# Optimization experiments

Measured on AMD Instinct MI355X. Metric: run time of the kernel, lower is better.

The kernel has to match this reference:

```python
import jax, jax.numpy as jnp
import numpy as np

B, NV, RN, SN = 1, 4, 1024, 128
H = W = 256
C_FEAT = 32   # img_feat_dim
D_VIEW = 32   # view transformer d_model
PE_D = 8      # PE_d_hid
D_RAY = D_VIEW + PE_D  # 40
NHEAD = 8
EPS_LN = 1e-5


def _layernorm(x, g, b):
    m = x.mean(-1, keepdims=True)
    v = ((x - m) ** 2).mean(-1, keepdims=True)
    return (x - m) * jax.lax.rsqrt(v + EPS_LN) * g + b


def _linear_attention(q, k, v):
    # LoFTR kernelized linear attention; q,k,v: (n, L, h, d)
    Q = jax.nn.elu(q) + 1.0
    K = jax.nn.elu(k) + 1.0
    L = v.shape[1]
    KV = jnp.einsum('nshd,nshv->nhdv', K, v / L)
    Z = 1.0 / (jnp.einsum('nlhd,nhd->nlh', Q, K.sum(axis=1)) + 1e-6)
    return jnp.einsum('nlhd,nhdv,nlh->nlhv', Q, KV, Z) * L


def _loftr_self_layer(x, Wq, Wk, Wv, Wm, g1, b1, W1, W2, g2, b2):
    # LoFTREncoderLayer with self-attention (x is both query and source)
    n, L, d = x.shape
    dim = d // NHEAD
    q = (x @ Wq).reshape(n, L, NHEAD, dim)
    k = (x @ Wk).reshape(n, L, NHEAD, dim)
    v = (x @ Wv).reshape(n, L, NHEAD, dim)
    msg = _linear_attention(q, k, v).reshape(n, L, d) @ Wm
    msg = _layernorm(msg, g1, b1)
    msg = jax.nn.relu(jnp.concatenate([x, msg], -1) @ W1) @ W2
    msg = _layernorm(msg, g2, b2)
    return x + msg


def _grid_sample_2d(img, pix):
    # img: (N,C,H,W); pix: (N,RN,SN,2) in pixel coords.
    # bilinear, align_corners=True, zero padding; mask = in-bounds.
    N, C, Hh, Ww = img.shape
    x, y = pix[..., 0], pix[..., 1]
    mask = ((x >= 0) & (x <= Ww - 1) & (y >= 0) & (y <= Hh - 1)).astype(img.dtype)
    x0 = jnp.floor(x)
    y0 = jnp.floor(y)
    flat = img.reshape(N, C, Hh * Ww)

    def gather(ix, iy):
        valid = ((ix >= 0) & (ix < Ww) & (iy >= 0) & (iy < Hh)).astype(img.dtype)
        idx = (jnp.clip(iy, 0, Hh - 1) * Ww + jnp.clip(ix, 0, Ww - 1)).astype(jnp.int32)
        out = jnp.take_along_axis(flat, idx.reshape(N, 1, -1), axis=2)
        return out.reshape(N, C, ix.shape[1], ix.shape[2]) * valid[:, None]

    wx1 = x - x0
    wy1 = y - y0
    out = (gather(x0, y0) * ((1 - wx1) * (1 - wy1))[:, None]
           + gather(x0 + 1, y0) * (wx1 * (1 - wy1))[:, None]
           + gather(x0, y0 + 1) * ((1 - wx1) * wy1)[:, None]
           + gather(x0 + 1, y0 + 1) * (wx1 * wy1)[:, None])
    return out, mask


def _order_posenc(d_hid, n):
    pos = np.arange(n)[:, None].astype(np.float64)
    j = np.arange(d_hid)[None, :]
    tab = pos / np.power(10000.0, 2 * (j // 2) / d_hid)
    tab[:, 0::2] = np.sin(tab[:, 0::2])
    tab[:, 1::2] = np.cos(tab[:, 1::2])
    return jnp.asarray(tab, dtype=jnp.float32)


def _forward(point3D, source_imgs, source_imgs_feat, ref_pose_inv, source_poses_inv,
             source_poses, view_token,
             vt_Wq, vt_Wk, vt_Wv, vt_Wm, vt_g1, vt_b1, vt_W1, vt_W2, vt_g2, vt_b2,
             rt_Wq, rt_Wk, rt_Wv, rt_Wm, rt_g1, rt_b1, rt_W1, rt_W2, rt_g2, rt_b2,
             dm_W1, dm_b1, dm_W2, dm_b2, dm_W3, dm_b3,
             rw_W1, rw_b1, rw_W2, rw_b2, rw_W3, rw_b3):
    b, nv, _, h, w = source_imgs.shape
    _, rn, sn, _ = point3D.shape

    # relative viewing directions (B,NV,RN,SN,3)
    v1 = point3D - ref_pose_inv[:, None, None, :3, -1]
    v2 = point3D[:, None] - source_poses_inv[:, :, None, None, :3, -1]
    v1 = v1 / jnp.linalg.norm(v1, axis=-1, keepdims=True)
    v2 = v2 / jnp.linalg.norm(v2, axis=-1, keepdims=True)
    dir_relative = v1[:, None] - v2

    # project points into all source views: (B,NV,3,RN,SN)
    pts_h = jnp.concatenate([point3D, jnp.ones_like(point3D[..., :1])], -1)
    pip = jnp.einsum('bnij,brsj->bnirs', source_poses, pts_h)[:, :, :3]
    mask_valid_depth = (pip[:, :, 2] > 0).astype(point3D.dtype)
    pix = pip[:, :, :2] / pip[:, :, 2:3]
    grid = jnp.moveaxis(pix, 2, -1).reshape(b * nv, rn, sn, 2)

    feat_s, mask = _grid_sample_2d(source_imgs_feat.reshape(b * nv, -1, h, w), grid)
    rgb_s, _ = _grid_sample_2d(source_imgs.reshape(b * nv, -1, h, w), grid)
    mask = mask.reshape(b, nv, rn, sn) * mask_valid_depth

    # per-point multi-view tokens: (B*RN*SN, NV, C)
    x = feat_s.reshape(b, nv, -1, rn, sn).transpose(0, 3, 4, 1, 2).reshape(b * rn * sn, nv, -1)
    tok = jnp.broadcast_to(view_token, (x.shape[0], 1, view_token.shape[-1]))
    x = jnp.concatenate([tok, x], axis=1)  # prepend view token -> L = NV+1
    x = _loftr_self_layer(x, vt_Wq, vt_Wk, vt_Wv, vt_Wm, vt_g1, vt_b1, vt_W1, vt_W2, vt_g2, vt_b2)

    x1 = jnp.moveaxis(x, 1, 0)          # (NV+1, B*RN*SN, C)
    view_feature = x1[1:]
    x = x1[0].reshape(b * rn, sn, -1)   # token output per sample along ray

    pe = _order_posenc(PE_D, sn)        # (SN, 8)
    x = jnp.concatenate([x, jnp.broadcast_to(pe, (b * rn, sn, PE_D))], -1)
    x = _loftr_self_layer(x, rt_Wq, rt_Wk, rt_Wv, rt_Wm, rt_g1, rt_b1, rt_W1, rt_W2, rt_g2, rt_b2)

    hdm = jax.nn.relu(x @ dm_W1 + dm_b1)
    hdm = jax.nn.relu(hdm @ dm_W2 + dm_b2)
    srdf = hdm @ dm_W3 + dm_b3           # (B*RN, SN, 1)

    # radiance blending weights over views
    vf = view_feature.reshape(nv, b, rn, sn, -1).transpose(1, 2, 3, 0, 4)  # (B,RN,SN,NV,C)
    dr = dir_relative.transpose(0, 2, 3, 1, 4)                             # (B,RN,SN,NV,3)
    xw = jnp.concatenate([vf, dr], -1)
    xw = jax.nn.relu(xw @ rw_W1 + rw_b1)
    xw = jax.nn.relu(xw @ rw_W2 + rw_b2)
    xw = xw @ rw_W3 + rw_b3                                                # (B,RN,SN,NV,1)
    m = mask.transpose(0, 2, 3, 1)[..., None]
    xw = jnp.where(m == 0, -1e9, xw)
    weight = jax.nn.softmax(xw, axis=-2)
    w_bn = weight[..., 0].transpose(0, 3, 1, 2)[:, :, None]                # (B,NV,1,RN,SN)
    radiance = (rgb_s.reshape(b, nv, 3, rn, sn) * w_bn).sum(axis=1)        # (B,3,RN,SN)
    radiance = radiance.transpose(0, 2, 3, 1).reshape(b * rn * sn, 3)
    return radiance, srdf, pip


def setup_inputs() -> dict:
    key = jax.random.key(0)
    ks = jax.random.split(key, 4)
    u = jax.random.uniform(ks[0], (B, RN, SN, 3), dtype=jnp.float32)
    point3D = jnp.concatenate([u[..., :2] - 0.5, u[..., 2:] + 1.0], -1)  # x,y in [-.5,.5], z in [1,2]
    source_imgs = jax.random.normal(ks[1], (B, NV, 3, H, W), dtype=jnp.float32) * 0.5
    source_imgs_feat = jax.random.normal(ks[2], (B, NV, C_FEAT, H, W), dtype=jnp.float32) * 0.5

    f = 200.0
    P = np.array([[f, 0, W / 2, 0], [0, f, H / 2, 0], [0, 0, 1, 0], [0, 0, 0, 1]], np.float32)
    source_poses = jnp.asarray(np.broadcast_to(P, (B, NV, 4, 4)).copy())
    ref_pose_inv = jnp.asarray(np.broadcast_to(np.eye(4, dtype=np.float32), (B, 4, 4)).copy())
    spi = np.broadcast_to(np.eye(4, dtype=np.float32), (B, NV, 4, 4)).copy()
    spi[:, :, 0, 3] = np.linspace(-0.2, 0.2, NV, dtype=np.float32)  # camera centers
    source_poses_inv = jnp.asarray(spi)

    pk = jax.random.split(ks[3], 20)

    def lin(k, i, o):
        return jax.random.normal(k, (i, o), dtype=jnp.float32) * 0.05

    d, dr = D_VIEW, D_RAY
    params = dict(
        view_token=jax.random.normal(pk[0], (1, d), dtype=jnp.float32),
        vt_Wq=lin(pk[1], d, d), vt_Wk=lin(pk[2], d, d), vt_Wv=lin(pk[3], d, d), vt_Wm=lin(pk[4], d, d),
        vt_g1=jnp.ones(d), vt_b1=jnp.zeros(d),
        vt_W1=lin(pk[5], 2 * d, 2 * d), vt_W2=lin(pk[6], 2 * d, d),
        vt_g2=jnp.ones(d), vt_b2=jnp.zeros(d),
        rt_Wq=lin(pk[7], dr, dr), rt_Wk=lin(pk[8], dr, dr), rt_Wv=lin(pk[9], dr, dr), rt_Wm=lin(pk[10], dr, dr),
        rt_g1=jnp.ones(dr), rt_b1=jnp.zeros(dr),
        rt_W1=lin(pk[11], 2 * dr, 2 * dr), rt_W2=lin(pk[12], 2 * dr, dr),
        rt_g2=jnp.ones(dr), rt_b2=jnp.zeros(dr),
        dm_W1=lin(pk[13], dr, 32), dm_b1=jnp.zeros(32),
        dm_W2=lin(pk[14], 32, 16), dm_b2=jnp.zeros(16),
        dm_W3=lin(pk[15], 16, 1), dm_b3=jnp.zeros(1),
        rw_W1=lin(pk[16], d + 3, 16), rw_b1=jnp.zeros(16),
        rw_W2=lin(pk[17], 16, 8), rw_b2=jnp.zeros(8),
        rw_W3=lin(pk[18], 8, 1), rw_b3=jnp.zeros(1),
    )
    out = dict(point3D=point3D, source_imgs=source_imgs, source_imgs_feat=source_imgs_feat,
               ref_pose_inv=ref_pose_inv, source_poses_inv=source_poses_inv,
               source_poses=source_poses)
    out.update(params)
    return out


def reference(point3D, source_imgs, source_imgs_feat, ref_pose_inv, source_poses_inv,
              source_poses, view_token,
              vt_Wq, vt_Wk, vt_Wv, vt_Wm, vt_g1, vt_b1, vt_W1, vt_W2, vt_g2, vt_b2,
              rt_Wq, rt_Wk, rt_Wv, rt_Wm, rt_g1, rt_b1, rt_W1, rt_W2, rt_g2, rt_b2,
              dm_W1, dm_b1, dm_W2, dm_b2, dm_W3, dm_b3,
              rw_W1, rw_b1, rw_W2, rw_b2, rw_W3, rw_b3):
    return _forward(point3D, source_imgs, source_imgs_feat, ref_pose_inv, source_poses_inv,
                    source_poses, view_token,
                    vt_Wq, vt_Wk, vt_Wv, vt_Wm, vt_g1, vt_b1, vt_W1, vt_W2, vt_g2, vt_b2,
                    rt_Wq, rt_Wk, rt_Wv, rt_Wm, rt_g1, rt_b1, rt_W1, rt_W2, rt_g2, rt_b2,
                    dm_W1, dm_b1, dm_W2, dm_b2, dm_W3, dm_b3,
                    rw_W1, rw_b1, rw_W2, rw_b2, rw_W3, rw_b3)
```

## Files before the change

### kernel.cpp

```cpp
#include <hip/hip_runtime.h>
#include <hip/hip_bf16.h>
#include <math.h>

#define NPTS   131072
#define NVIEW  4
#define IMH    256
#define IMW    256

#define WS_FEATT   0u
#define WS_IMGT    8388608u
#define WS_X1      9437184u
#define WS_XR      26214400u
#define WS_MSG     31457280u
#define WS_RGB     36700160u
#define WS_DIR     38273024u
#define WS_MASK    39845888u
#define WS_MSGV    40370176u

__device__ __forceinline__ float elup1(float t) { return t > 0.f ? t + 1.f : expf(t); }

__device__ __forceinline__ unsigned short f2bf(float f) {
    __hip_bfloat16 h = __float2bfloat16(f);
    return *(unsigned short*)&h;
}

__global__ __launch_bounds__(256) void k0_transpose(
    const float* __restrict__ feat, const float* __restrict__ img,
    float* __restrict__ featT, float* __restrict__ imgT)
{
    int tid = blockIdx.x * 256 + threadIdx.x;
    int v = tid >> 16, pix = tid & 65535;
    float buf[32];
#pragma unroll
    for (int c = 0; c < 32; ++c)
        buf[c] = feat[((size_t)(v * 32 + c) << 16) + pix];
    float4* dst = (float4*)(featT + ((size_t)tid << 5));
#pragma unroll
    for (int q = 0; q < 8; ++q)
        dst[q] = make_float4(buf[4*q], buf[4*q+1], buf[4*q+2], buf[4*q+3]);
    float4 rgb;
    rgb.x = img[((size_t)(v * 3 + 0) << 16) + pix];
    rgb.y = img[((size_t)(v * 3 + 1) << 16) + pix];
    rgb.z = img[((size_t)(v * 3 + 2) << 16) + pix];
    rgb.w = 0.f;
    *(float4*)(imgT + ((size_t)tid << 2)) = rgb;
}

__global__ __launch_bounds__(256) void k1_geom_sample(
    const float* __restrict__ p3d, const float* __restrict__ rpi,
    const float* __restrict__ spi, const float* __restrict__ sp,
    const float* __restrict__ featT, const float* __restrict__ imgT,
    float* __restrict__ x1, float* __restrict__ rgbw,
    float* __restrict__ dirw, float* __restrict__ maskw,
    float* __restrict__ outpip)
{
    int tid = blockIdx.x * 256 + threadIdx.x;
    int p = tid >> 2, v = tid & 3;
    float X = p3d[p * 3 + 0], Y = p3d[p * 3 + 1], Z = p3d[p * 3 + 2];

    float a0 = X - rpi[3], a1 = Y - rpi[7], a2 = Z - rpi[11];
    float na = sqrtf(a0 * a0 + a1 * a1 + a2 * a2);
    a0 /= na; a1 /= na; a2 /= na;
    const float* sv = spi + v * 16;
    float b0 = X - sv[3], b1 = Y - sv[7], b2 = Z - sv[11];
    float nb = sqrtf(b0 * b0 + b1 * b1 + b2 * b2);
    b0 /= nb; b1 /= nb; b2 /= nb;
    dirw[(size_t)p * 12 + v * 3 + 0] = a0 - b0;
    dirw[(size_t)p * 12 + v * 3 + 1] = a1 - b1;
    dirw[(size_t)p * 12 + v * 3 + 2] = a2 - b2;

    const float* P = sp + v * 16;
    float pip0 = P[0] * X + P[1] * Y + P[2]  * Z + P[3];
    float pip1 = P[4] * X + P[5] * Y + P[6]  * Z + P[7];
    float pip2 = P[8] * X + P[9] * Y + P[10] * Z + P[11];
    outpip[(size_t)(v * 3 + 0) * NPTS + p] = pip0;
    outpip[(size_t)(v * 3 + 1) * NPTS + p] = pip1;
    outpip[(size_t)(v * 3 + 2) * NPTS + p] = pip2;

    float gx = pip0 / pip2, gy = pip1 / pip2;
    float inb = (gx >= 0.f && gx <= 255.f && gy >= 0.f && gy <= 255.f) ? 1.f : 0.f;
    float mvd = pip2 > 0.f ? 1.f : 0.f;
    maskw[(size_t)p * 4 + v] = inb * mvd;

    float x0f = floorf(gx), y0f = floorf(gy);
    float wx = gx - x0f, wy = gy - y0f;
    int ix0 = (int)x0f, iy0 = (int)y0f;
    float tw[4] = { (1.f-wx)*(1.f-wy), wx*(1.f-wy), (1.f-wx)*wy, wx*wy };
    int tdx[4] = { 0, 1, 0, 1 };
    int tdy[4] = { 0, 0, 1, 1 };

    float facc[32];
#pragma unroll
    for (int c = 0; c < 32; ++c) facc[c] = 0.f;
    float r0 = 0.f, r1 = 0.f, r2 = 0.f;

#pragma unroll
    for (int tno = 0; tno < 4; ++tno) {
        int ix = ix0 + tdx[tno], iy = iy0 + tdy[tno];
        float valid = (ix >= 0 && ix < IMW && iy >= 0 && iy < IMH) ? 1.f : 0.f;
        int cx = min(max(ix, 0), IMW - 1), cy = min(max(iy, 0), IMH - 1);
        float wgt = tw[tno] * valid;
        size_t base = ((size_t)v << 16) + ((size_t)cy << 8) + (size_t)cx;
        const float4* fp = (const float4*)(featT + base * 32);
#pragma unroll
        for (int q = 0; q < 8; ++q) {
            float4 f4 = fp[q];
            facc[4*q+0] += f4.x * wgt; facc[4*q+1] += f4.y * wgt;
            facc[4*q+2] += f4.z * wgt; facc[4*q+3] += f4.w * wgt;
        }
        float4 rp = *(const float4*)(imgT + base * 4);
        r0 += rp.x * wgt; r1 += rp.y * wgt; r2 += rp.z * wgt;
    }

    float4* xd = (float4*)(x1 + ((size_t)p * 4 + v) * 32);
#pragma unroll
    for (int q = 0; q < 8; ++q)
        xd[q] = make_float4(facc[4*q], facc[4*q+1], facc[4*q+2], facc[4*q+3]);
    rgbw[(size_t)p * 12 + v * 3 + 0] = r0;
    rgbw[(size_t)p * 12 + v * 3 + 1] = r1;
    rgbw[(size_t)p * 12 + v * 3 + 2] = r2;
}

__device__ __forceinline__ void fma4(const float4 xv, const float* __restrict__ w,
                                     const int stride, float* __restrict__ acc)
{
#pragma unroll
    for (int j = 0; j < 32; ++j) acc[j] = fmaf(xv.x, w[j],            acc[j]);
#pragma unroll
    for (int j = 0; j < 32; ++j) acc[j] = fmaf(xv.y, w[stride + j],   acc[j]);
#pragma unroll
    for (int j = 0; j < 32; ++j) acc[j] = fmaf(xv.z, w[2*stride + j], acc[j]);
#pragma unroll
    for (int j = 0; j < 32; ++j) acc[j] = fmaf(xv.w, w[3*stride + j], acc[j]);
}

#define K2A_BLK  128
#define K2A_PTS  24
#define K2A_GRID ((NPTS + K2A_PTS - 1) / K2A_PTS)

__global__ __launch_bounds__(K2A_BLK) void k2a_attn1(
    const float* __restrict__ x1g, const float* __restrict__ vtok,
    const float* __restrict__ Wq, const float* __restrict__ Wk,
    const float* __restrict__ Wv, const float* __restrict__ Wm,
    const float* __restrict__ g1v, const float* __restrict__ b1v,
    unsigned int* __restrict__ msgv)
{
    __shared__ float wsm[4160];
    __shared__ float kv[8160];

    int t = threadIdx.x;
    for (int i = t; i < 1024; i += K2A_BLK) {
        wsm[i] = Wq[i]; wsm[1024 + i] = Wk[i];
        wsm[2048 + i] = Wv[i]; wsm[3072 + i] = Wm[i];
    }
    if (t < 32) { wsm[4096 + t] = g1v[t]; wsm[4128 + t] = b1v[t]; }
    __syncthreads();

    int pl = t / 5, l = t - pl * 5;
    bool act = (t < K2A_PTS * 5);
    if (!act) { pl = 0; l = 0; }
    int p = blockIdx.x * K2A_PTS + pl;
    bool valid = act && (p < NPTS);
    int pload = p < NPTS ? p : NPTS - 1;
    const float4* xsrc = (l == 0) ? (const float4*)vtok
                                  : (const float4*)(x1g + ((size_t)pload * 4 + (l - 1)) * 32);
    const int rowbase = (pl * 5 + l) * 68;

    {
        float acc[32];
#pragma unroll
        for (int j = 0; j < 32; ++j) acc[j] = 0.f;
        for (int g = 0; g < 8; ++g) fma4(xsrc[g], &wsm[1024 + g * 128], 32, acc);
        if (act) {
            float* krow = &kv[rowbase];
#pragma unroll
            for (int j = 0; j < 32; j += 4)
                *(float4*)&krow[j] = make_float4(elup1(acc[j]), elup1(acc[j+1]),
                                                 elup1(acc[j+2]), elup1(acc[j+3]));
        }
    }
    {
        float acc[32];
#pragma unroll
        for (int j = 0; j < 32; ++j) acc[j] = 0.f;
        for (int g = 0; g < 8; ++g) fma4(xsrc[g], &wsm[2048 + g * 128], 32, acc);
        if (act) {
            float* vrow = &kv[rowbase + 32];
#pragma unroll
            for (int j = 0; j < 32; j += 4)
                *(float4*)&vrow[j] = make_float4(acc[j], acc[j+1], acc[j+2], acc[j+3]);
        }
    }
    float qv[32];
    {
        float acc[32];
#pragma unroll
        for (int j = 0; j < 32; ++j) acc[j] = 0.f;
        for (int g = 0; g < 8; ++g) fma4(xsrc[g], &wsm[g * 128], 32, acc);
#pragma unroll
        for (int j = 0; j < 32; ++j) qv[j] = elup1(acc[j]);
    }
    __syncthreads();

    float macc[32];
#pragma unroll
    for (int j = 0; j < 32; ++j) macc[j] = 0.f;
    for (int h = 0; h < 8; ++h) {
        float kvm[16] = {0,0,0,0,0,0,0,0,0,0,0,0,0,0,0,0};
        float ks0 = 0.f, ks1 = 0.f, ks2 = 0.f, ks3 = 0.f;
#pragma unroll
        for (int l2 = 0; l2 < 5; ++l2) {
            const float* row = &kv[(pl * 5 + l2) * 68 + h * 4];
            float4 K4 = *(const float4*)row;
            float4 V4 = *(const float4*)(row + 32);
            kvm[0]  = fmaf(K4.x, V4.x, kvm[0]);  kvm[1]  = fmaf(K4.x, V4.y, kvm[1]);
            kvm[2]  = fmaf(K4.x, V4.z, kvm[2]);  kvm[3]  = fmaf(K4.x, V4.w, kvm[3]);
            kvm[4]  = fmaf(K4.y, V4.x, kvm[4]);  kvm[5]  = fmaf(K4.y, V4.y, kvm[5]);
            kvm[6]  = fmaf(K4.y, V4.z, kvm[6]);  kvm[7]  = fmaf(K4.y, V4.w, kvm[7]);
            kvm[8]  = fmaf(K4.z, V4.x, kvm[8]);  kvm[9]  = fmaf(K4.z, V4.y, kvm[9]);
            kvm[10] = fmaf(K4.z, V4.z, kvm[10]); kvm[11] = fmaf(K4.z, V4.w, kvm[11]);
            kvm[12] = fmaf(K4.w, V4.x, kvm[12]); kvm[13] = fmaf(K4.w, V4.y, kvm[13]);
            kvm[14] = fmaf(K4.w, V4.z, kvm[14]); kvm[15] = fmaf(K4.w, V4.w, kvm[15]);
            ks0 += K4.x; ks1 += K4.y; ks2 += K4.z; ks3 += K4.w;
        }
        float q0 = qv[h*4], q1 = qv[h*4+1], q2 = qv[h*4+2], q3 = qv[h*4+3];
        float den = 1e-6f + q0*ks0 + q1*ks1 + q2*ks2 + q3*ks3;
        float inv = 1.f / den;
        float o0 = (q0*kvm[0] + q1*kvm[4] + q2*kvm[8]  + q3*kvm[12]) * inv;
        float o1 = (q0*kvm[1] + q1*kvm[5] + q2*kvm[9]  + q3*kvm[13]) * inv;
        float o2 = (q0*kvm[2] + q1*kvm[6] + q2*kvm[10] + q3*kvm[14]) * inv;
        float o3 = (q0*kvm[3] + q1*kvm[7] + q2*kvm[11] + q3*kvm[15]) * inv;

        const float* wm = &wsm[3072 + h * 4 * 32];
#pragma unroll
        for (int j = 0; j < 32; ++j) macc[j] = fmaf(o0, wm[j],      macc[j]);
#pragma unroll
        for (int j = 0; j < 32; ++j) macc[j] = fmaf(o1, wm[32 + j], macc[j]);
#pragma unroll
        for (int j = 0; j < 32; ++j) macc[j] = fmaf(o2, wm[64 + j], macc[j]);
#pragma unroll
        for (int j = 0; j < 32; ++j) macc[j] = fmaf(o3, wm[96 + j], macc[j]);
    }

    if (valid) {
        float s1 = 0.f, s2 = 0.f;
#pragma unroll
        for (int j = 0; j < 32; ++j) { s1 += macc[j]; s2 += macc[j] * macc[j]; }
        float m  = s1 * (1.f / 32.f);
        float va = s2 * (1.f / 32.f) - m * m;
        float rs = rsqrtf(va + 1e-5f);
        size_t tk = (size_t)p * 5 + l;
        unsigned int* dst = msgv + tk * 16;
#pragma unroll
        for (int j = 0; j < 32; j += 2) {
            float v0 = (macc[j]   - m) * rs * wsm[4096 + j]   + wsm[4128 + j];
            float v1 = (macc[j+1] - m) * rs * wsm[4096 + j+1] + wsm[4128 + j+1];
            dst[j >> 1] = ((unsigned int)f2bf(v1) << 16) | (unsigned int)f2bf(v0);
        }
    }
}

#define K2B_BLK  128
#define K2B_GRID (NPTS * 5 / K2B_BLK)

__global__ __launch_bounds__(K2B_BLK) void k2b_ffn1(
    float* __restrict__ x1g, const float* __restrict__ vtok,
    const unsigned int* __restrict__ msgv,
    const float* __restrict__ W1, const float* __restrict__ W2,
    const float* __restrict__ g2v, const float* __restrict__ b2v,
    float* __restrict__ xr)
{
    __shared__ float wsm[6208];
    int t = threadIdx.x;
    for (int i = t; i < 4096; i += K2B_BLK) wsm[i] = W1[i];
    for (int i = t; i < 2048; i += K2B_BLK) wsm[4096 + i] = W2[i];
    if (t < 32) { wsm[6144 + t] = g2v[t]; wsm[6176 + t] = b2v[t]; }
    __syncthreads();

    int tid = blockIdx.x * K2B_BLK + t;
    int p = tid / 5, l = tid - p * 5;
    const float4* xsrc = (l == 0) ? (const float4*)vtok
                                  : (const float4*)(x1g + ((size_t)p * 4 + (l - 1)) * 32);
    float x[32];
#pragma unroll
    for (int g = 0; g < 8; ++g) {
        float4 v4 = xsrc[g];
        x[4*g] = v4.x; x[4*g+1] = v4.y; x[4*g+2] = v4.z; x[4*g+3] = v4.w;
    }
    float msg[32];
    {
        const unsigned int* src = msgv + (size_t)tid * 16;
#pragma unroll
        for (int j = 0; j < 32; j += 2) {
            unsigned int u = src[j >> 1];
            msg[j]   = __uint_as_float(u << 16);
            msg[j+1] = __uint_as_float(u & 0xffff0000u);
        }
    }

    float oacc[32];
#pragma unroll
    for (int j = 0; j < 32; ++j) oacc[j] = 0.f;
#pragma unroll
    for (int half = 0; half < 2; ++half) {
        const int j0 = half * 32;
        float hacc[32];
#pragma unroll
        for (int j = 0; j < 32; ++j) hacc[j] = 0.f;
        for (int g = 0; g < 8; ++g)
            fma4(make_float4(x[4*g], x[4*g+1], x[4*g+2], x[4*g+3]),
                 &wsm[(g * 4) * 64 + j0], 64, hacc);
        for (int g = 0; g < 8; ++g)
            fma4(make_float4(msg[4*g], msg[4*g+1], msg[4*g+2], msg[4*g+3]),
                 &wsm[(32 + g * 4) * 64 + j0], 64, hacc);
#pragma unroll
        for (int j = 0; j < 32; ++j) hacc[j] = fmaxf(hacc[j], 0.f);
        for (int g = 0; g < 8; ++g)
            fma4(make_float4(hacc[4*g], hacc[4*g+1], hacc[4*g+2], hacc[4*g+3]),
                 &wsm[4096 + (j0 + g * 4) * 32], 32, oacc);
    }

    float s1 = 0.f, s2 = 0.f;
#pragma unroll
    for (int j = 0; j < 32; ++j) { s1 += oacc[j]; s2 += oacc[j] * oacc[j]; }
    float m  = s1 * (1.f / 32.f);
    float va = s2 * (1.f / 32.f) - m * m;
    float rs = rsqrtf(va + 1e-5f);
    float y[32];
#pragma unroll
    for (int j = 0; j < 32; ++j)
        y[j] = x[j] + (oacc[j] - m) * rs * wsm[6144 + j] + wsm[6176 + j];

    if (l == 0) {
        float4* dst = (float4*)(xr + (size_t)p * 40);
#pragma unroll
        for (int g = 0; g < 8; ++g)
            dst[g] = make_float4(y[4*g], y[4*g+1], y[4*g+2], y[4*g+3]);
        int sidx = p & 127;
#pragma unroll
        for (int c = 0; c < 8; ++c) {
            float den = (c < 2) ? 1.f : (c < 4) ? 10.f : (c < 6) ? 100.f : 1000.f;
            float arg = (float)sidx / den;
            xr[(size_t)p * 40 + 32 + c] = (c & 1) ? cosf(arg) : sinf(arg);
        }
    } else {
        float4* dst = (float4*)(x1g + ((size_t)p * 4 + (l - 1)) * 32);
#pragma unroll
        for (int g = 0; g < 8; ++g)
            dst[g] = make_float4(y[4*g], y[4*g+1], y[4*g+2], y[4*g+3]);
    }
}

__global__ __launch_bounds__(320) void k3a_attn(
    const float* __restrict__ xr,
    const float* __restrict__ Wq, const float* __restrict__ Wk,
    const float* __restrict__ Wv, const float* __restrict__ Wm,
    const float* __restrict__ g1, const float* __restrict__ b1,
    float* __restrict__ msg)
{
    __shared__ float kb[5120];
    __shared__ float vb[5120];
    __shared__ float wb[1600];
    __shared__ float kvb[200];
    __shared__ float ksb[40];
    int t = threadIdx.x, r = blockIdx.x;
    const float* xbase = xr + (size_t)r * 5120;
    int lg = t / 40, c = t % 40;

    for (int i = t; i < 1600; i += 320) wb[i] = Wk[i];
    __syncthreads();
    {
        float acc[16];
#pragma unroll
        for (int i = 0; i < 16; ++i) acc[i] = 0.f;
        for (int kk = 0; kk < 40; ++kk) {
            float w = wb[kk * 40 + c];
#pragma unroll
            for (int i = 0; i < 16; ++i) acc[i] += xbase[(lg * 16 + i) * 40 + kk] * w;
        }
#pragma unroll
        for (int i = 0; i < 16; ++i) kb[(lg * 16 + i) * 40 + c] = elup1(acc[i]);
    }
    __syncthreads();
    for (int i = t; i < 1600; i += 320) wb[i] = Wv[i];
    __syncthreads();
    {
        float acc[16];
#pragma unroll
        for (int i = 0; i < 16; ++i) acc[i] = 0.f;
        for (int kk = 0; kk < 40; ++kk) {
            float w = wb[kk * 40 + c];
#pragma unroll
            for (int i = 0; i < 16; ++i) acc[i] += xbase[(lg * 16 + i) * 40 + kk] * w;
        }
#pragma unroll
        for (int i = 0; i < 16; ++i) vb[(lg * 16 + i) * 40 + c] = acc[i];
    }
    __syncthreads();
    if (t < 200) {
        int h = t / 25, e = (t / 5) % 5, d = t % 5;
        float kvv2 = 0.f, ks = 0.f;
        for (int s2 = 0; s2 < 128; ++s2) {
            float kvv = kb[s2 * 40 + h * 5 + e];
            float vv  = vb[s2 * 40 + h * 5 + d];
            kvv2 += kvv * vv; ks += kvv;
        }
        kvb[t] = kvv2;
        if (d == 0) ksb[h * 5 + e] = ks;
    }
    __syncthreads();
    for (int i = t; i < 1600; i += 320) wb[i] = Wq[i];
    __syncthreads();
    {
        float acc[16];
#pragma unroll
        for (int i = 0; i < 16; ++i) acc[i] = 0.f;
        for (int kk = 0; kk < 40; ++kk) {
            float w = wb[kk * 40 + c];
#pragma unroll
            for (int i = 0; i < 16; ++i) acc[i] += xbase[(lg * 16 + i) * 40 + kk] * w;
        }
#pragma unroll
        for (int i = 0; i < 16; ++i) kb[(lg * 16 + i) * 40 + c] = elup1(acc[i]);
    }
    __syncthreads();
    {
        int h = c / 5, d = c % 5;
#pragma unroll 4
        for (int i = 0; i < 16; ++i) {
            int l = lg * 16 + i;
            float den = 1e-6f, o = 0.f;
#pragma unroll
            for (int e = 0; e < 5; ++e) {
                float q = kb[l * 40 + h * 5 + e];
                den += q * ksb[h * 5 + e];
                o   += q * kvb[h * 25 + e * 5 + d];
            }
            vb[l * 40 + c] = o / den;
        }
    }
    __syncthreads();
    for (int i = t; i < 1600; i += 320) wb[i] = Wm[i];
    __syncthreads();
    {
        float acc[16];
#pragma unroll
        for (int i = 0; i < 16; ++i) acc[i] = 0.f;
        for (int kk = 0; kk < 40; ++kk) {
            float w = wb[kk * 40 + c];
#pragma unroll
            for (int i = 0; i < 16; ++i) acc[i] += vb[(lg * 16 + i) * 40 + kk] * w;
        }
#pragma unroll
        for (int i = 0; i < 16; ++i) kb[(lg * 16 + i) * 40 + c] = acc[i];
    }
    __syncthreads();
    if (t < 128) {
        float s1 = 0.f, s2v = 0.f;
        for (int j = 0; j < 40; ++j) { float x = kb[t * 40 + j]; s1 += x; s2v += x * x; }
        float m = s1 * (1.f / 40.f), va = s2v * (1.f / 40.f) - m * m;
        float rs = rsqrtf(va + 1e-5f);
        for (int j = 0; j < 40; ++j)
            msg[((size_t)r * 128 + t) * 40 + j] = (kb[t * 40 + j] - m) * rs * g1[j] + b1[j];
    }
}

__global__ __launch_bounds__(320) void k3b_ffn(
    float* __restrict__ xr, const float* __restrict__ msg,
    const float* __restrict__ W1, const float* __restrict__ W2,
    const float* __restrict__ g2, const float* __restrict__ b2)
{
    __shared__ float hb[10240];
    __shared__ float wb[3200];
    int t = threadIdx.x, r = blockIdx.x;
    int lg = t / 40, c = t % 40;
    const float* xbase = xr + (size_t)r * 5120;
    const float* mbase = msg + (size_t)r * 5120;

    float hA[16], hB[16];
#pragma unroll
    for (int i = 0; i < 16; ++i) { hA[i] = 0.f; hB[i] = 0.f; }

    for (int i = t; i < 3200; i += 320) wb[i] = W1[i];
    __syncthreads();
    for (int kk = 0; kk < 40; ++kk) {
        float wa = wb[kk * 80 + c], wbb = wb[kk * 80 + c + 40];
#pragma unroll
        for (int i = 0; i < 16; ++i) {
            float xv = xbase[(lg * 16 + i) * 40 + kk];
            hA[i] += xv * wa; hB[i] += xv * wbb;
        }
    }
    __syncthreads();
    for (int i = t; i < 3200; i += 320) wb[i] = W1[3200 + i];
    __syncthreads();
    for (int kk = 0; kk < 40; ++kk) {
        float wa = wb[kk * 80 + c], wbb = wb[kk * 80 + c + 40];
#pragma unroll
        for (int i = 0; i < 16; ++i) {
            float mv = mbase[(lg * 16 + i) * 40 + kk];
            hA[i] += mv * wa; hB[i] += mv * wbb;
        }
    }
#pragma unroll
    for (int i = 0; i < 16; ++i) {
        hb[(lg * 16 + i) * 80 + c]      = fmaxf(hA[i], 0.f);
        hb[(lg * 16 + i) * 80 + c + 40] = fmaxf(hB[i], 0.f);
    }
    __syncthreads();
    for (int i = t; i < 3200; i += 320) wb[i] = W2[i];
    __syncthreads();
    float oa[16];
#pragma unroll
    for (int i = 0; i < 16; ++i) oa[i] = 0.f;
    for (int kk = 0; kk < 80; ++kk) {
        float w = wb[kk * 40 + c];
#pragma unroll
        for (int i = 0; i < 16; ++i) oa[i] += hb[(lg * 16 + i) * 80 + kk] * w;
    }
    __syncthreads();
#pragma unroll
    for (int i = 0; i < 16; ++i) hb[(lg * 16 + i) * 40 + c] = oa[i];
    __syncthreads();
    if (t < 128) {
        float s1 = 0.f, s2v = 0.f;
        for (int j = 0; j < 40; ++j) { float x = hb[t * 40 + j]; s1 += x; s2v += x * x; }
        float m = s1 * (1.f / 40.f), va = s2v * (1.f / 40.f) - m * m;
        float rs = rsqrtf(va + 1e-5f);
        for (int j = 0; j < 40; ++j) {
            float y = xbase[t * 40 + j] + (hb[t * 40 + j] - m) * rs * g2[j] + b2[j];
            xr[(size_t)r * 5120 + t * 40 + j] = y;
        }
    }
}

__global__ __launch_bounds__(256) void k4_dm(
    const float* __restrict__ xr,
    const float* __restrict__ W1, const float* __restrict__ b1,
    const float* __restrict__ W2, const float* __restrict__ b2,
    const float* __restrict__ W3, const float* __restrict__ b3,
    float* __restrict__ out1)
{
    __shared__ float s[1857];
    int t = threadIdx.x;
    for (int i = t; i < 1280; i += 256) s[i] = W1[i];
    if (t < 32) s[1280 + t] = b1[t];
    for (int i = t; i < 512; i += 256) s[1312 + i] = W2[i];
    if (t < 16) { s[1824 + t] = b2[t]; s[1840 + t] = W3[t]; }
    if (t == 0) s[1856] = b3[0];
    __syncthreads();

    int p = blockIdx.x * 256 + t;
    float x[40];
    const float4* xp = (const float4*)(xr + (size_t)p * 40);
#pragma unroll
    for (int i = 0; i < 10; ++i) {
        float4 v4 = xp[i];
        x[4*i] = v4.x; x[4*i+1] = v4.y; x[4*i+2] = v4.z; x[4*i+3] = v4.w;
    }
    float h1[32];
#pragma unroll
    for (int j = 0; j < 32; ++j) h1[j] = s[1280 + j];
    for (int k = 0; k < 40; ++k) {
        float xv = x[k];
#pragma unroll
        for (int j = 0; j < 32; ++j) h1[j] += xv * s[k * 32 + j];
    }
#pragma unroll
    for (int j = 0; j < 32; ++j) h1[j] = fmaxf(h1[j], 0.f);
    float h2[16];
#pragma unroll
    for (int j = 0; j < 16; ++j) h2[j] = s[1824 + j];
    for (int k = 0; k < 32; ++k) {
        float hv = h1[k];
#pragma unroll
        for (int j = 0; j < 16; ++j) h2[j] += hv * s[1312 + k * 16 + j];
    }
    float o = s[1856];
#pragma unroll
    for (int j = 0; j < 16; ++j) o += fmaxf(h2[j], 0.f) * s[1840 + j];
    out1[p] = o;
}

__global__ __launch_bounds__(256) void k5_rw(
    const float* __restrict__ vf, const float* __restrict__ dirw,
    const float* __restrict__ maskw, const float* __restrict__ rgbw,
    const float* __restrict__ W1, const float* __restrict__ b1,
    const float* __restrict__ W2, const float* __restrict__ b2,
    const float* __restrict__ W3, const float* __restrict__ b3,
    float* __restrict__ out0)
{
    __shared__ float s[721];
    int t = threadIdx.x;
    for (int i = t; i < 560; i += 256) s[i] = W1[i];
    if (t < 16) s[560 + t] = b1[t];
    if (t < 128) s[576 + t] = W2[t];
    if (t < 8) { s[704 + t] = b2[t]; s[712 + t] = W3[t]; }
    if (t == 0) s[720] = b3[0];
    __syncthreads();

    int p = blockIdx.x * 256 + t;
    float xw[4];
#pragma unroll
    for (int v = 0; v < 4; ++v) {
        float in[35];
        const float4* vp = (const float4*)(vf + ((size_t)p * 4 + v) * 32);
#pragma unroll
        for (int q = 0; q < 8; ++q) {
            float4 f4 = vp[q];
            in[4*q] = f4.x; in[4*q+1] = f4.y; in[4*q+2] = f4.z; in[4*q+3] = f4.w;
        }
        in[32] = dirw[(size_t)p * 12 + v * 3 + 0];
        in[33] = dirw[(size_t)p * 12 + v * 3 + 1];
        in[34] = dirw[(size_t)p * 12 + v * 3 + 2];
        float h1[16];
#pragma unroll
        for (int j = 0; j < 16; ++j) h1[j] = s[560 + j];
        for (int k = 0; k < 35; ++k) {
            float xv = in[k];
#pragma unroll
            for (int j = 0; j < 16; ++j) h1[j] += xv * s[k * 16 + j];
        }
        float h2[8];
#pragma unroll
        for (int j = 0; j < 8; ++j) h2[j] = s[704 + j];
        for (int k = 0; k < 16; ++k) {
            float hv = fmaxf(h1[k], 0.f);
#pragma unroll
            for (int j = 0; j < 8; ++j) h2[j] += hv * s[576 + k * 8 + j];
        }
        float o = s[720];
#pragma unroll
        for (int j = 0; j < 8; ++j) o += fmaxf(h2[j], 0.f) * s[712 + j];
        xw[v] = (maskw[(size_t)p * 4 + v] == 0.f) ? -1e9f : o;
    }
    float m = fmaxf(fmaxf(xw[0], xw[1]), fmaxf(xw[2], xw[3]));
    float e0 = expf(xw[0] - m), e1 = expf(xw[1] - m), e2 = expf(xw[2] - m), e3 = expf(xw[3] - m);
    float inv = 1.f / (e0 + e1 + e2 + e3);
    float w4[4] = { e0 * inv, e1 * inv, e2 * inv, e3 * inv };
    float r0 = 0.f, r1 = 0.f, r2 = 0.f;
#pragma unroll
    for (int v = 0; v < 4; ++v) {
        r0 += rgbw[(size_t)p * 12 + v * 3 + 0] * w4[v];
        r1 += rgbw[(size_t)p * 12 + v * 3 + 1] * w4[v];
        r2 += rgbw[(size_t)p * 12 + v * 3 + 2] * w4[v];
    }
    out0[(size_t)p * 3 + 0] = r0;
    out0[(size_t)p * 3 + 1] = r1;
    out0[(size_t)p * 3 + 2] = r2;
}

extern "C" void kernel_launch(void* const* d_in, const int* in_sizes, int n_in,
                              void* d_out, int out_size, void* d_ws, size_t ws_size,
                              hipStream_t stream) {
    (void)in_sizes; (void)n_in; (void)out_size; (void)ws_size;
    const float* p3d   = (const float*)d_in[0];
    const float* imgs  = (const float*)d_in[1];
    const float* feat  = (const float*)d_in[2];
    const float* rpi   = (const float*)d_in[3];
    const float* spi   = (const float*)d_in[4];
    const float* sp    = (const float*)d_in[5];
    const float* vtok  = (const float*)d_in[6];
    const float* vtWq  = (const float*)d_in[7];
    const float* vtWk  = (const float*)d_in[8];
    const float* vtWv  = (const float*)d_in[9];
    const float* vtWm  = (const float*)d_in[10];
    const float* vtg1  = (const float*)d_in[11];
    const float* vtb1  = (const float*)d_in[12];
    const float* vtW1  = (const float*)d_in[13];
    const float* vtW2  = (const float*)d_in[14];
    const float* vtg2  = (const float*)d_in[15];
    const float* vtb2  = (const float*)d_in[16];
    const float* rtWq  = (const float*)d_in[17];
    const float* rtWk  = (const float*)d_in[18];
    const float* rtWv  = (const float*)d_in[19];
    const float* rtWm  = (const float*)d_in[20];
    const float* rtg1  = (const float*)d_in[21];
    const float* rtb1  = (const float*)d_in[22];
    const float* rtW1  = (const float*)d_in[23];
    const float* rtW2  = (const float*)d_in[24];
    const float* rtg2  = (const float*)d_in[25];
    const float* rtb2  = (const float*)d_in[26];
    const float* dmW1  = (const float*)d_in[27];
    const float* dmb1  = (const float*)d_in[28];
    const float* dmW2  = (const float*)d_in[29];
    const float* dmb2  = (const float*)d_in[30];
    const float* dmW3  = (const float*)d_in[31];
    const float* dmb3  = (const float*)d_in[32];
    const float* rwW1  = (const float*)d_in[33];
    const float* rwb1  = (const float*)d_in[34];
    const float* rwW2  = (const float*)d_in[35];
    const float* rwb2  = (const float*)d_in[36];
    const float* rwW3  = (const float*)d_in[37];
    const float* rwb3  = (const float*)d_in[38];

    float* out  = (float*)d_out;
    float* out0 = out;
    float* out1 = out + 393216;
    float* out2 = out + 524288;

    float* ws    = (float*)d_ws;
    float* featT = ws + WS_FEATT;
    float* imgT  = ws + WS_IMGT;
    float* x1    = ws + WS_X1;
    float* xr    = ws + WS_XR;
    float* msg   = ws + WS_MSG;
    float* rgbw  = ws + WS_RGB;
    float* dirw  = ws + WS_DIR;
    float* maskw = ws + WS_MASK;
    unsigned int* msgv = (unsigned int*)(ws + WS_MSGV);

    k0_transpose<<<dim3(1024), dim3(256), 0, stream>>>(feat, imgs, featT, imgT);
    k1_geom_sample<<<dim3(2048), dim3(256), 0, stream>>>(p3d, rpi, spi, sp, featT, imgT,
                                                         x1, rgbw, dirw, maskw, out2);
    k2a_attn1<<<dim3(K2A_GRID), dim3(K2A_BLK), 0, stream>>>(x1, vtok, vtWq, vtWk, vtWv, vtWm,
                                                            vtg1, vtb1, msgv);
    k2b_ffn1<<<dim3(K2B_GRID), dim3(K2B_BLK), 0, stream>>>(x1, vtok, msgv, vtW1, vtW2,
                                                           vtg2, vtb2, xr);
    k3a_attn<<<dim3(1024), dim3(320), 0, stream>>>(xr, rtWq, rtWk, rtWv, rtWm, rtg1, rtb1, msg);
    k3b_ffn<<<dim3(1024), dim3(320), 0, stream>>>(xr, msg, rtW1, rtW2, rtg2, rtb2);
    k4_dm<<<dim3(512), dim3(256), 0, stream>>>(xr, dmW1, dmb1, dmW2, dmb2, dmW3, dmb3, out1);
    k5_rw<<<dim3(512), dim3(256), 0, stream>>>(x1, dirw, maskw, rgbw,
                                               rwW1, rwb1, rwW2, rwb2, rwW3, rwb3, out0);
}
```

Baseline: 1.206 ms.

## Split ray attention into KV-reduction and per-point kernels with register-tiled matmuls

Ray-transformer attention is restructured. One kernel computes per-ray K/V projections and the KV and K-sum reductions into a small workspace. A second kernel does per-point Q projection, attention output, Wm projection and layernorm entirely in registers, and writes the message as bf16. The FFN kernel becomes one thread per point with all weights in shared memory, replacing the earlier per-column scheme that re-read x from global memory many times. k2b block size is also doubled. The trade-off is higher register pressure from 40-wide accumulators and reduced precision in the stored message.

```diff
diff --git a/kernel.cpp b/kernel.cpp
--- a/kernel.cpp
+++ b/kernel.cpp
@@ -16,6 +16,7 @@
 #define WS_DIR     38273024u
 #define WS_MASK    39845888u
 #define WS_MSGV    40370176u
+#define WS_RAYKV   (WS_MSG + 3000000u)
 
 __device__ __forceinline__ float elup1(float t) { return t > 0.f ? t + 1.f : expf(t); }
 
@@ -132,6 +133,19 @@
     for (int j = 0; j < 32; ++j) acc[j] = fmaf(xv.z, w[2*stride + j], acc[j]);
 #pragma unroll
     for (int j = 0; j < 32; ++j) acc[j] = fmaf(xv.w, w[3*stride + j], acc[j]);
+}
+
+__device__ __forceinline__ void fma40(const float4 xv, const float* __restrict__ w,
+                                      const int stride, float* __restrict__ acc)
+{
+#pragma unroll
+    for (int j = 0; j < 40; ++j) acc[j] = fmaf(xv.x, w[j],            acc[j]);
+#pragma unroll
+    for (int j = 0; j < 40; ++j) acc[j] = fmaf(xv.y, w[stride + j],   acc[j]);
+#pragma unroll
+    for (int j = 0; j < 40; ++j) acc[j] = fmaf(xv.z, w[2*stride + j], acc[j]);
+#pragma unroll
+    for (int j = 0; j < 40; ++j) acc[j] = fmaf(xv.w, w[3*stride + j], acc[j]);
 }
 
 #define K2A_BLK  128
@@ -260,7 +274,7 @@
     }
 }
 
-#define K2B_BLK  128
+#define K2B_BLK  256
 #define K2B_GRID (NPTS * 5 / K2B_BLK)
 
 __global__ __launch_bounds__(K2B_BLK) void k2b_ffn1(
@@ -351,187 +365,219 @@
     }
 }
 
-__global__ __launch_bounds__(320) void k3a_attn(
+#define K3A1_BLK 128
+
+__global__ __launch_bounds__(K3A1_BLK) void k3a1_kv(
     const float* __restrict__ xr,
-    const float* __restrict__ Wq, const float* __restrict__ Wk,
-    const float* __restrict__ Wv, const float* __restrict__ Wm,
+    const float* __restrict__ Wk, const float* __restrict__ Wv,
+    float* __restrict__ rayKV)
+{
+    __shared__ float wsm[3200];
+    __shared__ float rows[2 * 128 * 41];
+
+    int t = threadIdx.x, r = blockIdx.x;
+    for (int i = t; i < 1600; i += K3A1_BLK) { wsm[i] = Wk[i]; wsm[1600 + i] = Wv[i]; }
+
+    float x[40];
+    {
+        const float4* xp = (const float4*)(xr + ((size_t)r * 128 + t) * 40);
+#pragma unroll
+        for (int g = 0; g < 10; ++g) {
+            float4 v4 = xp[g];
+            x[4*g] = v4.x; x[4*g+1] = v4.y; x[4*g+2] = v4.z; x[4*g+3] = v4.w;
+        }
+    }
+    __syncthreads();
+
+    {
+        float acc[40];
+#pragma unroll
+        for (int j = 0; j < 40; ++j) acc[j] = 0.f;
+        for (int g = 0; g < 10; ++g)
+            fma40(make_float4(x[4*g], x[4*g+1], x[4*g+2], x[4*g+3]),
+                  &wsm[(4 * g) * 40], 40, acc);
+        float* kb = &rows[t * 41];
+#pragma unroll
+        for (int j = 0; j < 40; ++j) kb[j] = elup1(acc[j]);
+    }
+    {
+        float acc[40];
+#pragma unroll
+        for (int j = 0; j < 40; ++j) acc[j] = 0.f;
+        for (int g = 0; g < 10; ++g)
+            fma40(make_float4(x[4*g], x[4*g+1], x[4*g+2], x[4*g+3]),
+                  &wsm[1600 + (4 * g) * 40], 40, acc);
+        float* vb = &rows[5248 + t * 41];
+#pragma unroll
+        for (int j = 0; j < 40; ++j) vb[j] = acc[j];
+    }
+    __syncthreads();
+
+#pragma unroll
+    for (int phase = 0; phase < 2; ++phase) {
+        int c = t + phase * 128;
+        if (c < 200) {
+            int h = c / 25, e = (c / 5) % 5, d = c % 5;
+            float kvv = 0.f, ks = 0.f;
+            for (int s = 0; s < 128; ++s) {
+                float kf = rows[s * 41 + h * 5 + e];
+                float vf = rows[5248 + s * 41 + h * 5 + d];
+                kvv = fmaf(kf, vf, kvv); ks += kf;
+            }
+            rayKV[(size_t)r * 240 + c] = kvv;
+            if (d == 0) rayKV[(size_t)r * 240 + 200 + h * 5 + e] = ks;
+        }
+    }
+}
+
+#define K3A2_BLK 256
+
+__global__ __launch_bounds__(K3A2_BLK) void k3a2_qattn(
+    const float* __restrict__ xr, const float* __restrict__ rayKV,
+    const float* __restrict__ Wq, const float* __restrict__ Wm,
     const float* __restrict__ g1, const float* __restrict__ b1,
-    float* __restrict__ msg)
-{
-    __shared__ float kb[5120];
-    __shared__ float vb[5120];
-    __shared__ float wb[1600];
-    __shared__ float kvb[200];
-    __shared__ float ksb[40];
-    int t = threadIdx.x, r = blockIdx.x;
-    const float* xbase = xr + (size_t)r * 5120;
-    int lg = t / 40, c = t % 40;
-
-    for (int i = t; i < 1600; i += 320) wb[i] = Wk[i];
-    __syncthreads();
-    {
-        float acc[16];
-#pragma unroll
-        for (int i = 0; i < 16; ++i) acc[i] = 0.f;
-        for (int kk = 0; kk < 40; ++kk) {
-            float w = wb[kk * 40 + c];
-#pragma unroll
-            for (int i = 0; i < 16; ++i) acc[i] += xbase[(lg * 16 + i) * 40 + kk] * w;
-        }
-#pragma unroll
-        for (int i = 0; i < 16; ++i) kb[(lg * 16 + i) * 40 + c] = elup1(acc[i]);
-    }
-    __syncthreads();
-    for (int i = t; i < 1600; i += 320) wb[i] = Wv[i];
-    __syncthreads();
-    {
-        float acc[16];
-#pragma unroll
-        for (int i = 0; i < 16; ++i) acc[i] = 0.f;
-        for (int kk = 0; kk < 40; ++kk) {
-            float w = wb[kk * 40 + c];
-#pragma unroll
-            for (int i = 0; i < 16; ++i) acc[i] += xbase[(lg * 16 + i) * 40 + kk] * w;
-        }
-#pragma unroll
-        for (int i = 0; i < 16; ++i) vb[(lg * 16 + i) * 40 + c] = acc[i];
-    }
-    __syncthreads();
-    if (t < 200) {
-        int h = t / 25, e = (t / 5) % 5, d = t % 5;
-        float kvv2 = 0.f, ks = 0.f;
-        for (int s2 = 0; s2 < 128; ++s2) {
-            float kvv = kb[s2 * 40 + h * 5 + e];
-            float vv  = vb[s2 * 40 + h * 5 + d];
-            kvv2 += kvv * vv; ks += kvv;
-        }
-        kvb[t] = kvv2;
-        if (d == 0) ksb[h * 5 + e] = ks;
-    }
-    __syncthreads();
-    for (int i = t; i < 1600; i += 320) wb[i] = Wq[i];
-    __syncthreads();
-    {
-        float acc[16];
-#pragma unroll
-        for (int i = 0; i < 16; ++i) acc[i] = 0.f;
-        for (int kk = 0; kk < 40; ++kk) {
-            float w = wb[kk * 40 + c];
-#pragma unroll
-            for (int i = 0; i < 16; ++i) acc[i] += xbase[(lg * 16 + i) * 40 + kk] * w;
-        }
-#pragma unroll
-        for (int i = 0; i < 16; ++i) kb[(lg * 16 + i) * 40 + c] = elup1(acc[i]);
-    }
-    __syncthreads();
-    {
-        int h = c / 5, d = c % 5;
-#pragma unroll 4
-        for (int i = 0; i < 16; ++i) {
-            int l = lg * 16 + i;
-            float den = 1e-6f, o = 0.f;
-#pragma unroll
-            for (int e = 0; e < 5; ++e) {
-                float q = kb[l * 40 + h * 5 + e];
-                den += q * ksb[h * 5 + e];
-                o   += q * kvb[h * 25 + e * 5 + d];
-            }
-            vb[l * 40 + c] = o / den;
-        }
-    }
-    __syncthreads();
-    for (int i = t; i < 1600; i += 320) wb[i] = Wm[i];
-    __syncthreads();
-    {
-        float acc[16];
-#pragma unroll
-        for (int i = 0; i < 16; ++i) acc[i] = 0.f;
-        for (int kk = 0; kk < 40; ++kk) {
-            float w = wb[kk * 40 + c];
-#pragma unroll
-            for (int i = 0; i < 16; ++i) acc[i] += vb[(lg * 16 + i) * 40 + kk] * w;
-        }
-#pragma unroll
-        for (int i = 0; i < 16; ++i) kb[(lg * 16 + i) * 40 + c] = acc[i];
-    }
-    __syncthreads();
-    if (t < 128) {
-        float s1 = 0.f, s2v = 0.f;
-        for (int j = 0; j < 40; ++j) { float x = kb[t * 40 + j]; s1 += x; s2v += x * x; }
-        float m = s1 * (1.f / 40.f), va = s2v * (1.f / 40.f) - m * m;
-        float rs = rsqrtf(va + 1e-5f);
-        for (int j = 0; j < 40; ++j)
-            msg[((size_t)r * 128 + t) * 40 + j] = (kb[t * 40 + j] - m) * rs * g1[j] + b1[j];
-    }
-}
-
-__global__ __launch_bounds__(320) void k3b_ffn(
-    float* __restrict__ xr, const float* __restrict__ msg,
+    unsigned int* __restrict__ msgv2)
+{
+    __shared__ float wsm[3280];
+    int t = threadIdx.x;
+    for (int i = t; i < 1600; i += K3A2_BLK) { wsm[i] = Wq[i]; wsm[1600 + i] = Wm[i]; }
+    if (t < 40) { wsm[3200 + t] = g1[t]; wsm[3240 + t] = b1[t]; }
+    __syncthreads();
+
+    int tid = blockIdx.x * K3A2_BLK + t;
+    int r = tid >> 7;
+
+    float x[40];
+    {
+        const float4* xp = (const float4*)(xr + (size_t)tid * 40);
+#pragma unroll
+        for (int g = 0; g < 10; ++g) {
+            float4 v4 = xp[g];
+            x[4*g] = v4.x; x[4*g+1] = v4.y; x[4*g+2] = v4.z; x[4*g+3] = v4.w;
+        }
+    }
+    float q[40];
+    {
+        float acc[40];
+#pragma unroll
+        for (int j = 0; j < 40; ++j) acc[j] = 0.f;
+        for (int g = 0; g < 10; ++g)
+            fma40(make_float4(x[4*g], x[4*g+1], x[4*g+2], x[4*g+3]),
+                  &wsm[(4 * g) * 40], 40, acc);
+#pragma unroll
+        for (int j = 0; j < 40; ++j) q[j] = elup1(acc[j]);
+    }
+
+    const float* kvr = rayKV + (size_t)r * 240;
+    float ov[40];
+#pragma unroll
+    for (int h = 0; h < 8; ++h) {
+        float den = 1e-6f;
+#pragma unroll
+        for (int e = 0; e < 5; ++e) den = fmaf(q[h*5+e], kvr[200 + h*5 + e], den);
+        float inv = 1.f / den;
+#pragma unroll
+        for (int d = 0; d < 5; ++d) {
+            float o = 0.f;
+#pragma unroll
+            for (int e = 0; e < 5; ++e) o = fmaf(q[h*5+e], kvr[h*25 + e*5 + d], o);
+            ov[h*5+d] = o * inv;
+        }
+    }
+
+    float macc[40];
+#pragma unroll
+    for (int j = 0; j < 40; ++j) macc[j] = 0.f;
+    for (int g = 0; g < 10; ++g)
+        fma40(make_float4(ov[4*g], ov[4*g+1], ov[4*g+2], ov[4*g+3]),
+              &wsm[1600 + (4 * g) * 40], 40, macc);
+
+    float s1 = 0.f, s2 = 0.f;
+#pragma unroll
+    for (int j = 0; j < 40; ++j) { s1 += macc[j]; s2 += macc[j] * macc[j]; }
+    float m  = s1 * (1.f / 40.f);
+    float va = s2 * (1.f / 40.f) - m * m;
+    float rs = rsqrtf(va + 1e-5f);
+    unsigned int* dst = msgv2 + (size_t)tid * 20;
+#pragma unroll
+    for (int j = 0; j < 40; j += 2) {
+        float v0 = (macc[j]   - m) * rs * wsm[3200 + j]   + wsm[3240 + j];
+        float v1 = (macc[j+1] - m) * rs * wsm[3200 + j+1] + wsm[3240 + j+1];
+        dst[j >> 1] = ((unsigned int)f2bf(v1) << 16) | (unsigned int)f2bf(v0);
+    }
+}
+
+#define K3B_BLK 256
+
+__global__ __launch_bounds__(K3B_BLK) void k3b_ffn(
+    float* __restrict__ xr, const unsigned int* __restrict__ msgv2,
     const float* __restrict__ W1, const float* __restrict__ W2,
     const float* __restrict__ g2, const float* __restrict__ b2)
 {
-    __shared__ float hb[10240];
-    __shared__ float wb[3200];
-    int t = threadIdx.x, r = blockIdx.x;
-    int lg = t / 40, c = t % 40;
-    const float* xbase = xr + (size_t)r * 5120;
-    const float* mbase = msg + (size_t)r * 5120;
-
-    float hA[16], hB[16];
-#pragma unroll
-    for (int i = 0; i < 16; ++i) { hA[i] = 0.f; hB[i] = 0.f; }
-
-    for (int i = t; i < 3200; i += 320) wb[i] = W1[i];
-    __syncthreads();
-    for (int kk = 0; kk < 40; ++kk) {
-        float wa = wb[kk * 80 + c], wbb = wb[kk * 80 + c + 40];
-#pragma unroll
-        for (int i = 0; i < 16; ++i) {
-            float xv = xbase[(lg * 16 + i) * 40 + kk];
-            hA[i] += xv * wa; hB[i] += xv * wbb;
-        }
-    }
-    __syncthreads();
-    for (int i = t; i < 3200; i += 320) wb[i] = W1[3200 + i];
-    __syncthreads();
-    for (int kk = 0; kk < 40; ++kk) {
-        float wa = wb[kk * 80 + c], wbb = wb[kk * 80 + c + 40];
-#pragma unroll
-        for (int i = 0; i < 16; ++i) {
-            float mv = mbase[(lg * 16 + i) * 40 + kk];
-            hA[i] += mv * wa; hB[i] += mv * wbb;
-        }
-    }
-#pragma unroll
-    for (int i = 0; i < 16; ++i) {
-        hb[(lg * 16 + i) * 80 + c]      = fmaxf(hA[i], 0.f);
-        hb[(lg * 16 + i) * 80 + c + 40] = fmaxf(hB[i], 0.f);
-    }
-    __syncthreads();
-    for (int i = t; i < 3200; i += 320) wb[i] = W2[i];
-    __syncthreads();
-    float oa[16];
-#pragma unroll
-    for (int i = 0; i < 16; ++i) oa[i] = 0.f;
-    for (int kk = 0; kk < 80; ++kk) {
-        float w = wb[kk * 40 + c];
-#pragma unroll
-        for (int i = 0; i < 16; ++i) oa[i] += hb[(lg * 16 + i) * 80 + kk] * w;
-    }
-    __syncthreads();
-#pragma unroll
-    for (int i = 0; i < 16; ++i) hb[(lg * 16 + i) * 40 + c] = oa[i];
-    __syncthreads();
-    if (t < 128) {
-        float s1 = 0.f, s2v = 0.f;
-        for (int j = 0; j < 40; ++j) { float x = hb[t * 40 + j]; s1 += x; s2v += x * x; }
-        float m = s1 * (1.f / 40.f), va = s2v * (1.f / 40.f) - m * m;
-        float rs = rsqrtf(va + 1e-5f);
-        for (int j = 0; j < 40; ++j) {
-            float y = xbase[t * 40 + j] + (hb[t * 40 + j] - m) * rs * g2[j] + b2[j];
-            xr[(size_t)r * 5120 + t * 40 + j] = y;
-        }
-    }
+    __shared__ float wsm[9680];
+    int t = threadIdx.x;
+    for (int i = t; i < 6400; i += K3B_BLK) wsm[i] = W1[i];
+    for (int i = t; i < 3200; i += K3B_BLK) wsm[6400 + i] = W2[i];
+    if (t < 40) { wsm[9600 + t] = g2[t]; wsm[9640 + t] = b2[t]; }
+    __syncthreads();
+
+    int tid = blockIdx.x * K3B_BLK + t;
+    float x[40];
+    {
+        const float4* xp = (const float4*)(xr + (size_t)tid * 40);
+#pragma unroll
+        for (int g = 0; g < 10; ++g) {
+            float4 v4 = xp[g];
+            x[4*g] = v4.x; x[4*g+1] = v4.y; x[4*g+2] = v4.z; x[4*g+3] = v4.w;
+        }
+    }
+    float msg[40];
+    {
+        const unsigned int* src = msgv2 + (size_t)tid * 20;
+#pragma unroll
+        for (int j = 0; j < 40; j += 2) {
+            unsigned int u = src[j >> 1];
+            msg[j]   = __uint_as_float(u << 16);
+            msg[j+1] = __uint_as_float(u & 0xffff0000u);
+        }
+    }
+
+    float oacc[40];
+#pragma unroll
+    for (int j = 0; j < 40; ++j) oacc[j] = 0.f;
+#pragma unroll
+    for (int half = 0; half < 2; ++half) {
+        const int j0 = half * 40;
+        float hacc[40];
+#pragma unroll
+        for (int j = 0; j < 40; ++j) hacc[j] = 0.f;
+        for (int g = 0; g < 10; ++g)
+            fma40(make_float4(x[4*g], x[4*g+1], x[4*g+2], x[4*g+3]),
+                  &wsm[(4 * g) * 80 + j0], 80, hacc);
+        for (int g = 0; g < 10; ++g)
+            fma40(make_float4(msg[4*g], msg[4*g+1], msg[4*g+2], msg[4*g+3]),
+                  &wsm[(40 + 4 * g) * 80 + j0], 80, hacc);
+#pragma unroll
+        for (int j = 0; j < 40; ++j) hacc[j] = fmaxf(hacc[j], 0.f);
+        for (int g = 0; g < 10; ++g)
+            fma40(make_float4(hacc[4*g], hacc[4*g+1], hacc[4*g+2], hacc[4*g+3]),
+                  &wsm[6400 + (j0 + 4 * g) * 40], 40, oacc);
+    }
+
+    float s1 = 0.f, s2 = 0.f;
+#pragma unroll
+    for (int j = 0; j < 40; ++j) { s1 += oacc[j]; s2 += oacc[j] * oacc[j]; }
+    float m  = s1 * (1.f / 40.f);
+    float va = s2 * (1.f / 40.f) - m * m;
+    float rs = rsqrtf(va + 1e-5f);
+    float y[40];
+#pragma unroll
+    for (int j = 0; j < 40; ++j)
+        y[j] = x[j] + (oacc[j] - m) * rs * wsm[9600 + j] + wsm[9640 + j];
+    float4* dst = (float4*)(xr + (size_t)tid * 40);
+#pragma unroll
+    for (int g = 0; g < 10; ++g)
+        dst[g] = make_float4(y[4*g], y[4*g+1], y[4*g+2], y[4*g+3]);
 }
 
 __global__ __launch_bounds__(256) void k4_dm(
@@ -704,11 +750,12 @@
     float* imgT  = ws + WS_IMGT;
     float* x1    = ws + WS_X1;
     float* xr    = ws + WS_XR;
-    float* msg   = ws + WS_MSG;
     float* rgbw  = ws + WS_RGB;
     float* dirw  = ws + WS_DIR;
     float* maskw = ws + WS_MASK;
-    unsigned int* msgv = (unsigned int*)(ws + WS_MSGV);
+    unsigned int* msgv  = (unsigned int*)(ws + WS_MSGV);
+    unsigned int* msgv2 = (unsigned int*)(ws + WS_MSG);
+    float* rayKV = ws + WS_RAYKV;
 
     k0_transpose<<<dim3(1024), dim3(256), 0, stream>>>(feat, imgs, featT, imgT);
     k1_geom_sample<<<dim3(2048), dim3(256), 0, stream>>>(p3d, rpi, spi, sp, featT, imgT,
@@ -717,8 +764,10 @@
                                                             vtg1, vtb1, msgv);
     k2b_ffn1<<<dim3(K2B_GRID), dim3(K2B_BLK), 0, stream>>>(x1, vtok, msgv, vtW1, vtW2,
                                                            vtg2, vtb2, xr);
-    k3a_attn<<<dim3(1024), dim3(320), 0, stream>>>(xr, rtWq, rtWk, rtWv, rtWm, rtg1, rtb1, msg);
-    k3b_ffn<<<dim3(1024), dim3(320), 0, stream>>>(xr, msg, rtW1, rtW2, rtg2, rtb2);
+    k3a1_kv<<<dim3(1024), dim3(K3A1_BLK), 0, stream>>>(xr, rtWk, rtWv, rayKV);
+    k3a2_qattn<<<dim3(512), dim3(K3A2_BLK), 0, stream>>>(xr, rayKV, rtWq, rtWm,
+                                                         rtg1, rtb1, msgv2);
+    k3b_ffn<<<dim3(512), dim3(K3B_BLK), 0, stream>>>(xr, msgv2, rtW1, rtW2, rtg2, rtb2);
     k4_dm<<<dim3(512), dim3(256), 0, stream>>>(xr, dmW1, dmb1, dmW2, dmb2, dmW3, dmb3, out1);
     k5_rw<<<dim3(512), dim3(256), 0, stream>>>(x1, dirw, maskw, rgbw,
                                                rwW1, rwb1, rwW2, rwb2, rwW3, rwb3, out0);
```

Result: slower. 2.342 ms (+94.2%).
